# Performance work log

Hardware: AMD Instinct MI355X
Metric: run time of the kernel (lower is better)

Reference implementation:

```python
import jax, jax.numpy as jnp
import numpy as np

B, S, HID = 2, 512, 2048
HQ, HKV, D = 16, 4, 128
G = HQ // HKV
MAXP = 4096
PAST = 1536  # kv-cache start index (tokens already in cache)
EPS = 1e-6
NEG = -1e30


def _make_rope(past, s, d):
    half = d // 2
    inv_freq = 1.0 / (10000.0 ** (np.arange(half, dtype=np.float64) / half))
    pos = np.arange(past, past + s, dtype=np.float64)
    ang = pos[:, None] * inv_freq[None, :]
    return np.concatenate([np.cos(ang), np.sin(ang)], axis=-1).astype(np.float32)


def setup_inputs() -> dict:
    key = jax.random.key(0)
    ks = jax.random.split(key, 8)
    hidden_states = jax.random.normal(ks[0], (B, S, HID), jnp.float32)
    past_key_value = jax.random.normal(ks[1], (B, 2, HKV, MAXP, D), jnp.float32) * 0.5
    rope = jnp.broadcast_to(jnp.asarray(_make_rope(PAST, S, D))[None], (B, S, D))
    sc = 1.0 / np.sqrt(HID)
    Wq = jax.random.normal(ks[2], (HID, HQ * D), jnp.float32) * sc
    Wk = jax.random.normal(ks[3], (HID, HKV * D), jnp.float32) * sc
    Wv = jax.random.normal(ks[4], (HID, HKV * D), jnp.float32) * sc
    Wo = jax.random.normal(ks[5], (HQ * D, HID), jnp.float32) * (1.0 / np.sqrt(HQ * D))
    q_norm_w = jnp.ones((D,), jnp.float32)
    k_norm_w = jnp.ones((D,), jnp.float32)
    context_lengths = jnp.full((B,), PAST + S, jnp.int32)
    kvcache_start_index = jnp.full((1,), PAST, jnp.int32)
    return {"hidden_states": hidden_states, "past_key_value": past_key_value,
            "rope_rotary_cos_sin": rope, "Wq": Wq, "Wk": Wk, "Wv": Wv, "Wo": Wo,
            "q_norm_w": q_norm_w, "k_norm_w": k_norm_w,
            "context_lengths": context_lengths,
            "kvcache_start_index": kvcache_start_index}


def _rms_norm(x, w):
    # per-head RMSNorm over head_dim (Qwen3-style q_norm/k_norm)
    var = jnp.mean(jnp.square(x), axis=-1, keepdims=True)
    return x * jax.lax.rsqrt(var + EPS) * w


def _apply_rope(x, cos, sin):
    # x: [B,S,H,D]; cos/sin: [B,S,1,D/2] (neox-style half rotation)
    x1, x2 = jnp.split(x, 2, axis=-1)
    return jnp.concatenate([x1 * cos - x2 * sin, x2 * cos + x1 * sin], axis=-1)


def reference(hidden_states, past_key_value, rope_rotary_cos_sin,
              Wq, Wk, Wv, Wo, q_norm_w, k_norm_w,
              context_lengths, kvcache_start_index):
    bsz, q_len, _ = hidden_states.shape
    # QKV projections
    q = (hidden_states @ Wq).reshape(bsz, q_len, HQ, D)
    k = (hidden_states @ Wk).reshape(bsz, q_len, HKV, D)
    v = (hidden_states @ Wv).reshape(bsz, q_len, HKV, D)
    # per-head QK norm
    q = _rms_norm(q, q_norm_w)
    k = _rms_norm(k, k_norm_w)
    # RoPE (cos_sin: [B,S,D] = [cos(D/2) | sin(D/2)], fp32)
    cos = rope_rotary_cos_sin[..., : D // 2][:, :, None, :]
    sin = rope_rotary_cos_sin[..., D // 2:][:, :, None, :]
    q = _apply_rope(q, cos, sin)
    k = _apply_rope(k, cos, sin)
    # KV cache write at kvcache_start_index (in-place update, plugin semantics)
    start = kvcache_start_index[0]
    new_kv = jnp.stack([k.transpose(0, 2, 1, 3), v.transpose(0, 2, 1, 3)], axis=1)  # [B,2,HKV,S,D]
    present = jax.lax.dynamic_update_slice(
        past_key_value, new_kv.astype(past_key_value.dtype), (0, 0, 0, start, 0))
    ck = present[:, 0]  # [B,HKV,P,D]
    cv = present[:, 1]
    # GQA attention over the cache, causal w.r.t. absolute position
    qg = q.reshape(bsz, q_len, HKV, G, D).transpose(0, 2, 3, 1, 4)  # [B,HKV,G,S,D]
    scores = jnp.einsum('bhgsd,bhpd->bhgsp', qg, ck) / np.sqrt(D)
    kpos = jnp.arange(MAXP)
    limit = start + jnp.arange(q_len) + 1  # [S]: query i sees cache[0 : start+i+1]
    mask = (kpos[None, None, :] < limit[None, :, None]) & \
           (kpos[None, None, :] < context_lengths[:, None, None])  # [B,S,P]
    scores = jnp.where(mask[:, None, None], scores, NEG)
    probs = jax.nn.softmax(scores, axis=-1)
    out = jnp.einsum('bhgsp,bhpd->bhgsd', probs, cv)
    out = out.transpose(0, 3, 1, 2, 4).reshape(bsz, q_len, HQ * D)
    attn_output = out @ Wo
    return attn_output, present
```

## Files before the change

kernel.cpp:

```cpp
#include <hip/hip_runtime.h>

typedef unsigned short u16;
typedef unsigned int u32;
typedef __attribute__((ext_vector_type(4))) float f32x4;
typedef __attribute__((ext_vector_type(8))) __bf16 bf16x8;
typedef __attribute__((ext_vector_type(8))) unsigned short u16x8;

#define MAXP_ 4096
#define TOTROWS 16384
#define NCHUNK 4
#define NCALLOC 4
#define CHUNKP 512

__device__ __forceinline__ u16 f2bf(float f) {
    union { float f; u32 u; } x; x.f = f;
    u32 r = x.u + 0x7FFFu + ((x.u >> 16) & 1u);
    return (u16)(r >> 16);
}
__device__ __forceinline__ float bf2f(u16 u) {
    union { u32 u; float f; } x; x.u = ((u32)u) << 16; return x.f;
}
__device__ __forceinline__ u32 packbf(float lo, float hi) {
    return (u32)f2bf(lo) | ((u32)f2bf(hi) << 16);
}
__device__ __forceinline__ u32 bperm(int addr, u32 src) {
    return (u32)__builtin_amdgcn_ds_bpermute(addr, (int)src);
}

#define GLOAD16(g, l) __builtin_amdgcn_global_load_lds( \
    (const __attribute__((address_space(1))) void*)(g), \
    (__attribute__((address_space(3))) void*)(l), 16, 0, 0)

__global__ __launch_bounds__(256) void prep(const float* __restrict__ hidden,
        const float* __restrict__ Wq, const float* __restrict__ Wk, const float* __restrict__ Wv,
        u16* __restrict__ hb, u16* __restrict__ Wqkvt) {
    const int bid = blockIdx.x;
    const int t = threadIdx.x;
    if (bid < 1024) {
        int i = bid * 256 + t;
        const float* s = hidden + (long)i * 8;
        f32x4 a = *(const f32x4*)s;
        f32x4 b = *(const f32x4*)(s + 4);
        u16x8 o;
#pragma unroll
        for (int j = 0; j < 4; ++j) { o[j] = f2bf(a[j]); o[4 + j] = f2bf(b[j]); }
        *(u16x8*)&hb[(long)i * 8] = o;
        return;
    }
    __shared__ __align__(16) u16 T[64][72];
    const float* W; int N_w, n_off, n0, k0;
    if (bid < 2048)      { int b2 = bid - 1024; W = Wq; N_w = 2048; n_off = 0;    n0 = (b2 & 31) * 64; k0 = (b2 >> 5) * 64; }
    else if (bid < 2304) { int b2 = bid - 2048; W = Wk; N_w = 512;  n_off = 2048; n0 = (b2 & 7) * 64;  k0 = (b2 >> 3) * 64; }
    else                 { int b2 = bid - 2304; W = Wv; N_w = 512;  n_off = 2560; n0 = (b2 & 7) * 64;  k0 = (b2 >> 3) * 64; }
    {
        int r = t >> 2, c4 = (t & 3) * 16;
        const float* src = W + (long)(k0 + r) * N_w + n0 + c4;
        f32x4 a0 = *(const f32x4*)src, a1 = *(const f32x4*)(src + 4);
        f32x4 a2 = *(const f32x4*)(src + 8), a3 = *(const f32x4*)(src + 12);
        u16x8 p0, p1;
#pragma unroll
        for (int j = 0; j < 4; ++j) {
            p0[j] = f2bf(a0[j]); p0[4 + j] = f2bf(a1[j]);
            p1[j] = f2bf(a2[j]); p1[4 + j] = f2bf(a3[j]);
        }
        *(u16x8*)&T[r][c4] = p0;
        *(u16x8*)&T[r][c4 + 8] = p1;
    }
    __syncthreads();
    {
        int n = t >> 2, k4 = (t & 3) * 16;
        u16x8 q0, q1;
#pragma unroll
        for (int j = 0; j < 8; ++j) { q0[j] = T[k4 + j][n]; q1[j] = T[k4 + 8 + j][n]; }
        u16* dst = Wqkvt + (long)(n_off + n0 + n) * 2048 + k0 + k4;
        *(u16x8*)dst = q0;
        *(u16x8*)(dst + 8) = q1;
    }
}

__global__ __launch_bounds__(256) void trans_w(const float* __restrict__ W, u16* __restrict__ Wt,
                                               int N_w, int K, int n_off) {
    __shared__ __align__(16) u16 T[64][72];
    const int t = threadIdx.x;
    const int n0 = blockIdx.x * 64, k0 = blockIdx.y * 64;
    {
        int r = t >> 2, c4 = (t & 3) * 16;
        const float* src = W + (long)(k0 + r) * N_w + n0 + c4;
        f32x4 a0 = *(const f32x4*)src, a1 = *(const f32x4*)(src + 4);
        f32x4 a2 = *(const f32x4*)(src + 8), a3 = *(const f32x4*)(src + 12);
        u16x8 p0, p1;
#pragma unroll
        for (int j = 0; j < 4; ++j) {
            p0[j] = f2bf(a0[j]); p0[4 + j] = f2bf(a1[j]);
            p1[j] = f2bf(a2[j]); p1[4 + j] = f2bf(a3[j]);
        }
        *(u16x8*)&T[r][c4] = p0;
        *(u16x8*)&T[r][c4 + 8] = p1;
    }
    __syncthreads();
    {
        int n = t >> 2, k4 = (t & 3) * 16;
        u16x8 q0, q1;
#pragma unroll
        for (int j = 0; j < 8; ++j) { q0[j] = T[k4 + j][n]; q1[j] = T[k4 + 8 + j][n]; }
        u16* dst = Wt + (long)(n_off + n0 + n) * K + k0 + k4;
        *(u16x8*)dst = q0;
        *(u16x8*)(dst + 8) = q1;
    }
}

__global__ __launch_bounds__(256) void copy_past2(const float* __restrict__ past,
        float* __restrict__ present, u16* __restrict__ Kc, u16* __restrict__ Vtc,
        const int* __restrict__ startp, const int* __restrict__ ctxp) {
    __shared__ __align__(16) u16 T[128][72];
    const int bkh = blockIdx.y;
    const int b = bkh >> 3, kv = (bkh >> 2) & 1, h = bkh & 3;
    const int p0 = blockIdx.x * 64;
    const int t = threadIdx.x;
    const int p = t >> 2, d0 = (t & 3) * 32;
    const float* src = past + ((long)bkh * MAXP_ + p0 + p) * 128 + d0;
    float* dst = present + ((long)bkh * MAXP_ + p0 + p) * 128 + d0;
    f32x4 v[8];
#pragma unroll
    for (int j = 0; j < 8; ++j) { v[j] = *(const f32x4*)(src + j * 4); *(f32x4*)(dst + j * 4) = v[j]; }
    int klim = startp[0] + 512;
    int cx = ctxp[b];
    if (klim > cx) klim = cx;
    if (p0 >= klim) return;
    if (kv == 0) {
        u16* kd = Kc + ((long)(b * 4 + h) * MAXP_ + p0 + p) * 128 + d0;
#pragma unroll
        for (int j2 = 0; j2 < 4; ++j2) {
            u16x8 o;
#pragma unroll
            for (int e = 0; e < 4; ++e) { o[e] = f2bf(v[j2 * 2][e]); o[4 + e] = f2bf(v[j2 * 2 + 1][e]); }
            *(u16x8*)&kd[j2 * 8] = o;
        }
    } else {
#pragma unroll
        for (int j = 0; j < 8; ++j)
#pragma unroll
            for (int e = 0; e < 4; ++e)
                T[d0 + j * 4 + e][p] = f2bf(v[j][e]);
        __syncthreads();
        int d = t >> 1, pc = (t & 1) * 32;
        u16* vd = Vtc + ((long)(b * 4 + h) * 128 + d) * MAXP_ + p0 + pc;
#pragma unroll
        for (int j = 0; j < 4; ++j)
            *(u16x8*)&vd[j * 8] = *(const u16x8*)&T[d][pc + j * 8];
    }
}

__global__ __launch_bounds__(256) void gemm64(const u16* __restrict__ A, const u16* __restrict__ Bt,
                                              float* __restrict__ C, int M, int N, int K) {
    __shared__ __align__(16) u16 As0[4096], Bs0[4096], As1[4096], Bs1[4096];
    const int tid = threadIdx.x, lane = tid & 63, w = tid >> 6;
    const int wm = w >> 1, wn = w & 1;
    const int l15 = lane & 15, g = lane >> 4;
    const int m0 = blockIdx.y * 64, n0 = blockIdx.x * 64;
    f32x4 acc[2][2] = {};

    const int lrow = lane >> 3;
    const int sch = (lane & 7) ^ lrow;
    const int c0 = w, c1 = w + 4;
    const u16* ga0 = A + (long)(m0 + c0 * 8 + lrow) * K + sch * 8;
    const u16* ga1 = A + (long)(m0 + c1 * 8 + lrow) * K + sch * 8;
    const u16* gb0 = Bt + (long)(n0 + c0 * 8 + lrow) * K + sch * 8;
    const u16* gb1 = Bt + (long)(n0 + c1 * 8 + lrow) * K + sch * 8;
    const int ra = wm * 32, rb = wn * 32;
    const int h7 = l15 & 7;

#define STAGE_T(koff, AS_, BS_) do { \
        GLOAD16(ga0 + (koff), &AS_[c0 * 512]); \
        GLOAD16(ga1 + (koff), &AS_[c1 * 512]); \
        GLOAD16(gb0 + (koff), &BS_[c0 * 512]); \
        GLOAD16(gb1 + (koff), &BS_[c1 * 512]); \
    } while (0)

    auto compute = [&](const u16* as_, const u16* bs_) {
        bf16x8 af[2][2], bfr[2][2];
#pragma unroll
        for (int i = 0; i < 2; ++i) {
            int rr = ra + i * 16 + l15;
#pragma unroll
            for (int kk = 0; kk < 2; ++kk)
                af[i][kk] = *(const bf16x8*)&as_[rr * 64 + (((kk * 4 + g) ^ h7) * 8)];
        }
#pragma unroll
        for (int j = 0; j < 2; ++j) {
            int rr = rb + j * 16 + l15;
#pragma unroll
            for (int kk = 0; kk < 2; ++kk)
                bfr[j][kk] = *(const bf16x8*)&bs_[rr * 64 + (((kk * 4 + g) ^ h7) * 8)];
        }
#pragma unroll
        for (int i = 0; i < 2; ++i)
#pragma unroll
            for (int j = 0; j < 2; ++j) {
                acc[i][j] = __builtin_amdgcn_mfma_f32_16x16x32_bf16(af[i][0], bfr[j][0], acc[i][j], 0, 0, 0);
                acc[i][j] = __builtin_amdgcn_mfma_f32_16x16x32_bf16(af[i][1], bfr[j][1], acc[i][j], 0, 0, 0);
            }
    };

    STAGE_T(0, As0, Bs0);
    for (int k0 = 0; k0 < K; k0 += 128) {
        STAGE_T(k0 + 64, As1, Bs1);
        asm volatile("s_waitcnt vmcnt(4)" ::: "memory");
        __builtin_amdgcn_s_barrier();
        __builtin_amdgcn_sched_barrier(0);
        compute(As0, Bs0);
        __builtin_amdgcn_s_barrier();
        if (k0 + 128 < K) {
            STAGE_T(k0 + 128, As0, Bs0);
            asm volatile("s_waitcnt vmcnt(4)" ::: "memory");
        } else {
            asm volatile("s_waitcnt vmcnt(0)" ::: "memory");
        }
        __builtin_amdgcn_s_barrier();
        __builtin_amdgcn_sched_barrier(0);
        compute(As1, Bs1);
        __builtin_amdgcn_s_barrier();
    }
#undef STAGE_T

#pragma unroll
    for (int i = 0; i < 2; ++i)
#pragma unroll
        for (int j = 0; j < 2; ++j)
#pragma unroll
            for (int r = 0; r < 4; ++r)
                C[(long)(m0 + ra + i * 16 + g * 4 + r) * N + n0 + rb + j * 16 + l15] = acc[i][j][r];
}

__global__ __launch_bounds__(256) void normrope_v(const float* __restrict__ QKVf,
        const float* __restrict__ rope,
        const float* __restrict__ qw, const float* __restrict__ kw,
        const int* __restrict__ startp, float* __restrict__ present,
        u16* __restrict__ Qn, u16* __restrict__ Kc, u16* __restrict__ Vtc) {
    const int bid = blockIdx.x;
    const int start = startp[0];
    if (bid < 6144) {
        const int wid = bid * 4 + (threadIdx.x >> 6);
        const int lane = threadIdx.x & 63;
        if (wid < 16384) {
            int row = wid >> 4, h = wid & 15;
            int b = row >> 9, s = row & 511;
            const float* src = QKVf + (long)row * 3072 + h * 128;
            float x1 = src[lane], x2 = src[64 + lane];
            float v = x1 * x1 + x2 * x2;
#pragma unroll
            for (int off = 32; off; off >>= 1) v += __shfl_xor(v, off, 64);
            float sc = rsqrtf(v * (1.0f / 128.0f) + 1e-6f);
            float y1 = x1 * sc * qw[lane], y2 = x2 * sc * qw[64 + lane];
            float c = rope[(long)row * 128 + lane], sn = rope[(long)row * 128 + 64 + lane];
            u16* dst = Qn + (((long)(b * 16 + h) * 512 + s) * 128);
            dst[lane] = f2bf(y1 * c - y2 * sn);
            dst[64 + lane] = f2bf(y2 * c + y1 * sn);
        } else if (wid < 20480) {
            int j = wid - 16384;
            int row = j >> 2, h = j & 3;
            int b = row >> 9, s = row & 511;
            const float* src = QKVf + (long)row * 3072 + 2048 + h * 128;
            float x1 = src[lane], x2 = src[64 + lane];
            float v = x1 * x1 + x2 * x2;
#pragma unroll
            for (int off = 32; off; off >>= 1) v += __shfl_xor(v, off, 64);
            float sc = rsqrtf(v * (1.0f / 128.0f) + 1e-6f);
            float y1 = x1 * sc * kw[lane], y2 = x2 * sc * kw[64 + lane];
            float c = rope[(long)row * 128 + lane], sn = rope[(long)row * 128 + 64 + lane];
            float k1 = y1 * c - y2 * sn, k2 = y2 * c + y1 * sn;
            float* dst = present + (((long)(b * 2 + 0) * 4 + h) * MAXP_ + (start + s)) * 128;
            dst[lane] = k1; dst[64 + lane] = k2;
            u16* kc = Kc + (((long)(b * 4 + h)) * MAXP_ + start + s) * 128;
            kc[lane] = f2bf(k1); kc[64 + lane] = f2bf(k2);
        } else if (wid < 24576) {
            int j = wid - 20480;
            int row = j >> 2, h = j & 3;
            int b = row >> 9, s = row & 511;
            const float* src = QKVf + (long)row * 3072 + 2560 + h * 128;
            float* dst = present + (((long)(b * 2 + 1) * 4 + h) * MAXP_ + (start + s)) * 128;
            dst[lane] = src[lane];
            dst[64 + lane] = src[64 + lane];
        }
        return;
    }
    __shared__ __align__(16) u16 T[128][72];
    const int t = threadIdx.x;
    const int b2 = bid - 6144;
    const int s0 = (b2 & 7) * 64;
    const int bh = b2 >> 3, b = bh >> 2, h = bh & 3;
    const int sr = t >> 2, d0 = (t & 3) * 32;
    const float* src = QKVf + (long)(b * 512 + s0 + sr) * 3072 + 2560 + h * 128 + d0;
#pragma unroll
    for (int j = 0; j < 8; ++j) {
        f32x4 v = *(const f32x4*)(src + j * 4);
#pragma unroll
        for (int e = 0; e < 4; ++e) T[d0 + j * 4 + e][sr] = f2bf(v[e]);
    }
    __syncthreads();
    const int d = t >> 1, pc = (t & 1) * 32;
    u16* dst = Vtc + ((long)(b * 4 + h) * 128 + d) * MAXP_ + start + s0 + pc;
#pragma unroll
    for (int k = 0; k < 32; ++k) dst[k] = T[d][pc + k];
}

__global__ __launch_bounds__(512, 4) void attn(const u16* __restrict__ Qn,
        const u16* __restrict__ Kc, const u16* __restrict__ Vtc,
        const int* __restrict__ startp, const int* __restrict__ ctxp,
        u16* __restrict__ op, float* __restrict__ mp, float* __restrict__ lp) {
    __shared__ __align__(16) char KsB[2][16384];
    __shared__ __align__(16) char VsB[2][16384];
    const int tid = threadIdx.x, lane = tid & 63, w = tid >> 6;
    const int l15 = lane & 15, g = lane >> 4;
    const bool ghi = (g >= 2);
    const int id = blockIdx.x;
    const int bh = id & 7;
    const int rest = id >> 3;
    const int c = rest >> 4;
    const int q0 = (rest & 15) * 32;
    const int b = bh >> 2, hkv = bh & 3;
    const int hd = w & 3, qh = w >> 2;
    const int hq = hkv * 4 + hd;
    const int start = startp[0];
    const int ctx = ctxp[b];

    int lim_blk = start + q0 + 32;
    if (lim_blk > ctx) lim_blk = ctx;
    const int pbeg = c * CHUNKP;
    int pend = pbeg + CHUNKP;
    if (pend > lim_blk) pend = lim_blk;
    if (pbeg >= pend) return;

    const int qrow0 = q0 + qh * 16;
    const long rowbase = (long)(b * 16 + hq) * 512 + qrow0;

    bf16x8 qb[4];
    {
        const u16* qp = Qn + (rowbase + l15) * 128 + g * 8;
#pragma unroll
        for (int kf = 0; kf < 4; ++kf)
            qb[kf] = *(const bf16x8*)(qp + kf * 32);
    }

    const char* kb8 = (const char*)(Kc + (long)bh * (MAXP_ * 128));
    const char* vb8 = (const char*)(Vtc + (long)bh * (128 * MAXP_));

    const int wbase = (tid & ~63) * 16;
    auto STAGE = [&](int buf, int p0_) {
#pragma unroll
        for (int r = 0; r < 2; ++r) {
            int o_ = r * 8192 + tid * 16;
            int row = o_ >> 8;
            int colb = (o_ & 255) ^ ((row & 7) << 4);
            GLOAD16(kb8 + (long)(p0_ + row) * 256 + colb, &KsB[buf][r * 8192 + wbase]);
        }
#pragma unroll
        for (int r = 0; r < 2; ++r) {
            int o_ = r * 8192 + tid * 16;
            int row = o_ >> 7;
            int colb = (o_ & 127) ^ ((row & 7) << 4);
            GLOAD16(vb8 + (long)row * (MAXP_ * 2) + (long)p0_ * 2 + colb, &VsB[buf][r * 8192 + wbase]);
        }
    };

    f32x4 o[8] = {};
    float m_run = -1e30f, l_run = 0.f;
    int limq = start + qrow0 + l15 + 1;
    if (limq > ctx) limq = ctx;
    if (limq > pend) limq = pend;
    const int addrA = (l15 + ((g & 1) << 5)) << 2;
    const int addrB = addrA + 64;
    const float scale = 0.08838834764831845f;
    const int swz = (l15 & 7) << 4;

    const int t0 = pbeg >> 6, t1 = (pend + 63) >> 6;
    STAGE(0, t0 * 64);
    asm volatile("s_waitcnt vmcnt(0)" ::: "memory");
    __builtin_amdgcn_s_barrier();
    int cur = 0;
    for (int t = t0; t < t1; ++t) {
        const int p0 = t * 64;
        if (t + 1 < t1) STAGE(cur ^ 1, p0 + 64);
        f32x4 sacc[4] = {};
#pragma unroll
        for (int kt = 0; kt < 4; ++kt) {
            const char* krow = &KsB[cur][(kt * 16 + l15) * 256];
#pragma unroll
            for (int kf = 0; kf < 4; ++kf) {
                bf16x8 ka = *(const bf16x8*)(krow + ((kf * 64 + g * 16) ^ swz));
                sacc[kt] = __builtin_amdgcn_mfma_f32_16x16x32_bf16(ka, qb[kf], sacc[kt], 0, 0, 0);
            }
        }
        float mx = -1e30f;
#pragma unroll
        for (int kt = 0; kt < 4; ++kt)
#pragma unroll
            for (int r = 0; r < 4; ++r) {
                int key = p0 + kt * 16 + g * 4 + r;
                float x = (key < limq) ? sacc[kt][r] * scale : -1e30f;
                sacc[kt][r] = x;
                mx = fmaxf(mx, x);
            }
        mx = fmaxf(mx, __shfl_xor(mx, 16, 64));
        mx = fmaxf(mx, __shfl_xor(mx, 32, 64));
        if (!__all(mx <= m_run + 8.f)) {
            float mnew = fmaxf(m_run, mx);
            float alpha = __expf(m_run - mnew);
            m_run = mnew;
            l_run *= alpha;
            f32x4 av;
#pragma unroll
            for (int r = 0; r < 4; ++r) av[r] = __shfl(alpha, g * 4 + r, 64);
#pragma unroll
            for (int df = 0; df < 8; ++df) {
                o[df][0] *= av[0]; o[df][1] *= av[1];
                o[df][2] *= av[2]; o[df][3] *= av[3];
            }
        }
        const float mb = m_run;
        float rs = 0.f;
        u32 w0[4], w1[4];
#pragma unroll
        for (int kt = 0; kt < 4; ++kt) {
#pragma unroll
            for (int r = 0; r < 4; ++r) {
                float p = __expf(sacc[kt][r] - mb);
                sacc[kt][r] = p;
                rs += p;
            }
            w0[kt] = packbf(sacc[kt][0], sacc[kt][1]);
            w1[kt] = packbf(sacc[kt][2], sacc[kt][3]);
        }
        rs += __shfl_xor(rs, 16, 64);
        rs += __shfl_xor(rs, 32, 64);
        l_run += rs;
#pragma unroll
        for (int ks = 0; ks < 2; ++ks) {
            const int sL = 2 * ks, sH = 2 * ks + 1;
            u32 d0 = ghi ? bperm(addrA, w0[sH]) : bperm(addrA, w0[sL]);
            u32 d1 = ghi ? bperm(addrA, w1[sH]) : bperm(addrA, w1[sL]);
            u32 d2 = ghi ? bperm(addrB, w0[sH]) : bperm(addrB, w0[sL]);
            u32 d3 = ghi ? bperm(addrB, w1[sH]) : bperm(addrB, w1[sL]);
            union { u32 d[4]; bf16x8 v; } pu;
            pu.d[0] = d0; pu.d[1] = d1; pu.d[2] = d2; pu.d[3] = d3;
            bf16x8 pa = pu.v;
#pragma unroll
            for (int df = 0; df < 8; ++df) {
                const char* vrow = &VsB[cur][(df * 16 + l15) * 128];
                bf16x8 vb = *(const bf16x8*)(vrow + ((ks * 64 + g * 16) ^ swz));
                o[df] = __builtin_amdgcn_mfma_f32_16x16x32_bf16(pa, vb, o[df], 0, 0, 0);
            }
        }
        asm volatile("s_waitcnt vmcnt(0)" ::: "memory");
        __builtin_amdgcn_s_barrier();
        cur ^= 1;
    }
    {
        float invl = l_run > 0.f ? 1.0f / l_run : 0.f;
        f32x4 iv;
#pragma unroll
        for (int r = 0; r < 4; ++r) iv[r] = __shfl(invl, g * 4 + r, 64);
        u16* dst = op + ((long)c * TOTROWS + rowbase + g * 4) * 128 + l15;
#pragma unroll
        for (int r = 0; r < 4; ++r)
#pragma unroll
            for (int df = 0; df < 8; ++df)
                dst[(long)r * 128 + df * 16] = f2bf(o[df][r] * iv[r]);
        if (g == 0) {
            mp[(long)c * TOTROWS + rowbase + l15] = m_run;
            lp[(long)c * TOTROWS + rowbase + l15] = l_run;
        }
    }
}

__global__ __launch_bounds__(256) void combine(const u16* __restrict__ op,
        const float* __restrict__ mp, const float* __restrict__ lp,
        const int* __restrict__ startp, const int* __restrict__ ctxp,
        u16* __restrict__ Af) {
    const int w = threadIdx.x >> 6, lane = threadIdx.x & 63;
    const long row = (long)blockIdx.x * 4 + w;
    const int b = (int)(row >> 13), hq = ((int)row >> 9) & 15, s = (int)row & 511;
    const int start = startp[0];
    int lim = start + s + 1;
    int cx = ctxp[b];
    if (lim > cx) lim = cx;
    float mc[NCALLOC], lc[NCALLOC];
    bool has[NCALLOC];
    float M = -1e30f;
#pragma unroll
    for (int c = 0; c < NCALLOC; ++c) {
        has[c] = (c * CHUNKP < lim);
        if (has[c]) {
            mc[c] = mp[(long)c * TOTROWS + row];
            lc[c] = lp[(long)c * TOTROWS + row];
            if (lc[c] > 0.f && mc[c] > M) M = mc[c];
        }
    }
    const int d0 = lane * 2;
    float Wt = 0.f, a0 = 0.f, a1 = 0.f;
#pragma unroll
    for (int c = 0; c < NCALLOC; ++c) {
        if (has[c] && lc[c] > 0.f) {
            float wg = lc[c] * __expf(mc[c] - M);
            Wt += wg;
            u32 pr = *(const u32*)&op[((long)c * TOTROWS + row) * 128 + d0];
            a0 += wg * bf2f((u16)(pr & 0xFFFF));
            a1 += wg * bf2f((u16)(pr >> 16));
        }
    }
    float inv = 1.0f / Wt;
    u32 pk = (u32)f2bf(a0 * inv) | ((u32)f2bf(a1 * inv) << 16);
    *(u32*)&Af[((long)(b * 512 + s) * 2048) + hq * 128 + d0] = pk;
}

extern "C" void kernel_launch(void* const* d_in, const int* in_sizes, int n_in,
                              void* d_out, int out_size, void* d_ws, size_t ws_size,
                              hipStream_t stream) {
    const float* hidden = (const float*)d_in[0];
    const float* past   = (const float*)d_in[1];
    const float* rope   = (const float*)d_in[2];
    const float* Wq     = (const float*)d_in[3];
    const float* Wk     = (const float*)d_in[4];
    const float* Wv     = (const float*)d_in[5];
    const float* Wo     = (const float*)d_in[6];
    const float* qw     = (const float*)d_in[7];
    const float* kw     = (const float*)d_in[8];
    const int*   ctx    = (const int*)d_in[9];
    const int*   start  = (const int*)d_in[10];

    float* out = (float*)d_out;
    float* present = out + 2097152;
    u16* Kc = (u16*)d_out;

    char* wsb = (char*)d_ws;
    u16*   hb    = (u16*)(wsb + 0);
    u16*   Wqkvt = (u16*)(wsb + 4194304);
    float* QKVf  = (float*)(wsb + 16777216);
    u16*   op    = (u16*)(wsb + 0);
    float* mp    = (float*)(wsb + 16777216);
    float* lp    = (float*)(wsb + 17039360);
    u16*   Wot   = (u16*)(wsb + 17301504);
    u16*   Qn    = (u16*)(wsb + 29360128);
    u16*   Af    = (u16*)(wsb + 29360128);
    u16*   Vtc   = (u16*)(wsb + 33554432);

    prep<<<dim3(2560), dim3(256), 0, stream>>>(hidden, Wq, Wk, Wv, hb, Wqkvt);
    copy_past2<<<dim3(64, 16), dim3(256), 0, stream>>>(past, present, Kc, Vtc, start, ctx);
    gemm64<<<dim3(48, 16), dim3(256), 0, stream>>>(hb, Wqkvt, QKVf, 1024, 3072, 2048);
    normrope_v<<<dim3(6208), dim3(256), 0, stream>>>(QKVf, rope, qw, kw, start, present, Qn, Kc, Vtc);
    trans_w<<<dim3(32, 32), dim3(256), 0, stream>>>(Wo, Wot, 2048, 2048, 0);
    attn<<<dim3(512), dim3(512), 0, stream>>>(Qn, Kc, Vtc, start, ctx, op, mp, lp);
    combine<<<dim3(4096), dim3(256), 0, stream>>>(op, mp, lp, start, ctx, Af);
    gemm64<<<dim3(32, 16), dim3(256), 0, stream>>>(Af, Wot, out, 1024, 2048, 2048);
}
```

Measured before the change: 130.1 us.

## Fuse KV-cache copy and Wo transpose into prep; XCD-aware GEMM tile mapping

Merges the past-cache copy/convert kernel and, when the workspace is large enough, the Wo transpose into the single prep launch. This cuts kernel launches and lets these independent memory-bound jobs run concurrently. The GEMM grid is flattened to 1D and blocks are remapped so each XCD handles a contiguous set of N tiles, aiming for better L2 locality. Risks include larger per-block shared memory in prep, which can lower occupancy, and a dependence on workspace size to choose the path.

```diff
diff --git a/kernel.cpp b/kernel.cpp
--- a/kernel.cpp
+++ b/kernel.cpp
@@ -33,7 +33,10 @@
 
 __global__ __launch_bounds__(256) void prep(const float* __restrict__ hidden,
         const float* __restrict__ Wq, const float* __restrict__ Wk, const float* __restrict__ Wv,
-        u16* __restrict__ hb, u16* __restrict__ Wqkvt) {
+        const float* __restrict__ Wo, const float* __restrict__ past,
+        u16* __restrict__ hb, u16* __restrict__ Wqkvt, u16* __restrict__ Wot,
+        float* __restrict__ present, u16* __restrict__ Kc, u16* __restrict__ Vtc,
+        const int* __restrict__ startp, const int* __restrict__ ctxp) {
     const int bid = blockIdx.x;
     const int t = threadIdx.x;
     if (bid < 1024) {
@@ -47,11 +50,52 @@
         *(u16x8*)&hb[(long)i * 8] = o;
         return;
     }
+    if (bid >= 2560 && bid < 3584) {
+        __shared__ __align__(16) u16 T[128][72];
+        const int b2 = bid - 2560;
+        const int bkh = b2 >> 6;
+        const int p0 = (b2 & 63) * 64;
+        const int b = bkh >> 3, kv = (bkh >> 2) & 1, h = bkh & 3;
+        const int p = t >> 2, d0 = (t & 3) * 32;
+        const float* src = past + ((long)bkh * MAXP_ + p0 + p) * 128 + d0;
+        float* dst = present + ((long)bkh * MAXP_ + p0 + p) * 128 + d0;
+        f32x4 v[8];
+#pragma unroll
+        for (int j = 0; j < 8; ++j) { v[j] = *(const f32x4*)(src + j * 4); *(f32x4*)(dst + j * 4) = v[j]; }
+        int klim = startp[0] + 512;
+        int cx = ctxp[b];
+        if (klim > cx) klim = cx;
+        if (p0 >= klim) return;
+        if (kv == 0) {
+            u16* kd = Kc + ((long)(b * 4 + h) * MAXP_ + p0 + p) * 128 + d0;
+#pragma unroll
+            for (int j2 = 0; j2 < 4; ++j2) {
+                u16x8 o;
+#pragma unroll
+                for (int e = 0; e < 4; ++e) { o[e] = f2bf(v[j2 * 2][e]); o[4 + e] = f2bf(v[j2 * 2 + 1][e]); }
+                *(u16x8*)&kd[j2 * 8] = o;
+            }
+        } else {
+#pragma unroll
+            for (int j = 0; j < 8; ++j)
+#pragma unroll
+                for (int e = 0; e < 4; ++e)
+                    T[d0 + j * 4 + e][p] = f2bf(v[j][e]);
+            __syncthreads();
+            int d = t >> 1, pc = (t & 1) * 32;
+            u16* vd = Vtc + ((long)(b * 4 + h) * 128 + d) * MAXP_ + p0 + pc;
+#pragma unroll
+            for (int j = 0; j < 4; ++j)
+                *(u16x8*)&vd[j * 8] = *(const u16x8*)&T[d][pc + j * 8];
+        }
+        return;
+    }
     __shared__ __align__(16) u16 T[64][72];
-    const float* W; int N_w, n_off, n0, k0;
-    if (bid < 2048)      { int b2 = bid - 1024; W = Wq; N_w = 2048; n_off = 0;    n0 = (b2 & 31) * 64; k0 = (b2 >> 5) * 64; }
-    else if (bid < 2304) { int b2 = bid - 2048; W = Wk; N_w = 512;  n_off = 2048; n0 = (b2 & 7) * 64;  k0 = (b2 >> 3) * 64; }
-    else                 { int b2 = bid - 2304; W = Wv; N_w = 512;  n_off = 2560; n0 = (b2 & 7) * 64;  k0 = (b2 >> 3) * 64; }
+    const float* W; u16* Wdst; int N_w, n_off, n0, k0;
+    if (bid < 2048)      { int b2 = bid - 1024; W = Wq; Wdst = Wqkvt; N_w = 2048; n_off = 0;    n0 = (b2 & 31) * 64; k0 = (b2 >> 5) * 64; }
+    else if (bid < 2304) { int b2 = bid - 2048; W = Wk; Wdst = Wqkvt; N_w = 512;  n_off = 2048; n0 = (b2 & 7) * 64;  k0 = (b2 >> 3) * 64; }
+    else if (bid < 2560) { int b2 = bid - 2304; W = Wv; Wdst = Wqkvt; N_w = 512;  n_off = 2560; n0 = (b2 & 7) * 64;  k0 = (b2 >> 3) * 64; }
+    else                 { int b2 = bid - 3584; W = Wo; Wdst = Wot;   N_w = 2048; n_off = 0;    n0 = (b2 & 31) * 64; k0 = (b2 >> 5) * 64; }
     {
         int r = t >> 2, c4 = (t & 3) * 16;
         const float* src = W + (long)(k0 + r) * N_w + n0 + c4;
@@ -72,7 +116,7 @@
         u16x8 q0, q1;
 #pragma unroll
         for (int j = 0; j < 8; ++j) { q0[j] = T[k4 + j][n]; q1[j] = T[k4 + 8 + j][n]; }
-        u16* dst = Wqkvt + (long)(n_off + n0 + n) * 2048 + k0 + k4;
+        u16* dst = Wdst + (long)(n_off + n0 + n) * 2048 + k0 + k4;
         *(u16x8*)dst = q0;
         *(u16x8*)(dst + 8) = q1;
     }
@@ -109,55 +153,15 @@
     }
 }
 
-__global__ __launch_bounds__(256) void copy_past2(const float* __restrict__ past,
-        float* __restrict__ present, u16* __restrict__ Kc, u16* __restrict__ Vtc,
-        const int* __restrict__ startp, const int* __restrict__ ctxp) {
-    __shared__ __align__(16) u16 T[128][72];
-    const int bkh = blockIdx.y;
-    const int b = bkh >> 3, kv = (bkh >> 2) & 1, h = bkh & 3;
-    const int p0 = blockIdx.x * 64;
-    const int t = threadIdx.x;
-    const int p = t >> 2, d0 = (t & 3) * 32;
-    const float* src = past + ((long)bkh * MAXP_ + p0 + p) * 128 + d0;
-    float* dst = present + ((long)bkh * MAXP_ + p0 + p) * 128 + d0;
-    f32x4 v[8];
-#pragma unroll
-    for (int j = 0; j < 8; ++j) { v[j] = *(const f32x4*)(src + j * 4); *(f32x4*)(dst + j * 4) = v[j]; }
-    int klim = startp[0] + 512;
-    int cx = ctxp[b];
-    if (klim > cx) klim = cx;
-    if (p0 >= klim) return;
-    if (kv == 0) {
-        u16* kd = Kc + ((long)(b * 4 + h) * MAXP_ + p0 + p) * 128 + d0;
-#pragma unroll
-        for (int j2 = 0; j2 < 4; ++j2) {
-            u16x8 o;
-#pragma unroll
-            for (int e = 0; e < 4; ++e) { o[e] = f2bf(v[j2 * 2][e]); o[4 + e] = f2bf(v[j2 * 2 + 1][e]); }
-            *(u16x8*)&kd[j2 * 8] = o;
-        }
-    } else {
-#pragma unroll
-        for (int j = 0; j < 8; ++j)
-#pragma unroll
-            for (int e = 0; e < 4; ++e)
-                T[d0 + j * 4 + e][p] = f2bf(v[j][e]);
-        __syncthreads();
-        int d = t >> 1, pc = (t & 1) * 32;
-        u16* vd = Vtc + ((long)(b * 4 + h) * 128 + d) * MAXP_ + p0 + pc;
-#pragma unroll
-        for (int j = 0; j < 4; ++j)
-            *(u16x8*)&vd[j * 8] = *(const u16x8*)&T[d][pc + j * 8];
-    }
-}
-
 __global__ __launch_bounds__(256) void gemm64(const u16* __restrict__ A, const u16* __restrict__ Bt,
                                               float* __restrict__ C, int M, int N, int K) {
     __shared__ __align__(16) u16 As0[4096], Bs0[4096], As1[4096], Bs1[4096];
     const int tid = threadIdx.x, lane = tid & 63, w = tid >> 6;
     const int wm = w >> 1, wn = w & 1;
     const int l15 = lane & 15, g = lane >> 4;
-    const int m0 = blockIdx.y * 64, n0 = blockIdx.x * 64;
+    const int ntile = N >> 6, npx = ntile >> 3;
+    const int xcd = blockIdx.x & 7, j_ = blockIdx.x >> 3;
+    const int m0 = (j_ / npx) * 64, n0 = (xcd * npx + j_ % npx) * 64;
     f32x4 acc[2][2] = {};
 
     const int lrow = lane >> 3;
@@ -187,18 +191,18 @@
                 af[i][kk] = *(const bf16x8*)&as_[rr * 64 + (((kk * 4 + g) ^ h7) * 8)];
         }
 #pragma unroll
-        for (int j = 0; j < 2; ++j) {
-            int rr = rb + j * 16 + l15;
+        for (int j2 = 0; j2 < 2; ++j2) {
+            int rr = rb + j2 * 16 + l15;
 #pragma unroll
             for (int kk = 0; kk < 2; ++kk)
-                bfr[j][kk] = *(const bf16x8*)&bs_[rr * 64 + (((kk * 4 + g) ^ h7) * 8)];
+                bfr[j2][kk] = *(const bf16x8*)&bs_[rr * 64 + (((kk * 4 + g) ^ h7) * 8)];
         }
 #pragma unroll
         for (int i = 0; i < 2; ++i)
 #pragma unroll
-            for (int j = 0; j < 2; ++j) {
-                acc[i][j] = __builtin_amdgcn_mfma_f32_16x16x32_bf16(af[i][0], bfr[j][0], acc[i][j], 0, 0, 0);
-                acc[i][j] = __builtin_amdgcn_mfma_f32_16x16x32_bf16(af[i][1], bfr[j][1], acc[i][j], 0, 0, 0);
+            for (int j2 = 0; j2 < 2; ++j2) {
+                acc[i][j2] = __builtin_amdgcn_mfma_f32_16x16x32_bf16(af[i][0], bfr[j2][0], acc[i][j2], 0, 0, 0);
+                acc[i][j2] = __builtin_amdgcn_mfma_f32_16x16x32_bf16(af[i][1], bfr[j2][1], acc[i][j2], 0, 0, 0);
             }
     };
 
@@ -226,10 +230,10 @@
 #pragma unroll
     for (int i = 0; i < 2; ++i)
 #pragma unroll
-        for (int j = 0; j < 2; ++j)
+        for (int j2 = 0; j2 < 2; ++j2)
 #pragma unroll
             for (int r = 0; r < 4; ++r)
-                C[(long)(m0 + ra + i * 16 + g * 4 + r) * N + n0 + rb + j * 16 + l15] = acc[i][j][r];
+                C[(long)(m0 + ra + i * 16 + g * 4 + r) * N + n0 + rb + j2 * 16 + l15] = acc[i][j2][r];
 }
 
 __global__ __launch_bounds__(256) void normrope_v(const float* __restrict__ QKVf,
@@ -539,17 +543,28 @@
     u16*   op    = (u16*)(wsb + 0);
     float* mp    = (float*)(wsb + 16777216);
     float* lp    = (float*)(wsb + 17039360);
-    u16*   Wot   = (u16*)(wsb + 17301504);
     u16*   Qn    = (u16*)(wsb + 29360128);
     u16*   Af    = (u16*)(wsb + 29360128);
     u16*   Vtc   = (u16*)(wsb + 33554432);
-
-    prep<<<dim3(2560), dim3(256), 0, stream>>>(hidden, Wq, Wk, Wv, hb, Wqkvt);
-    copy_past2<<<dim3(64, 16), dim3(256), 0, stream>>>(past, present, Kc, Vtc, start, ctx);
-    gemm64<<<dim3(48, 16), dim3(256), 0, stream>>>(hb, Wqkvt, QKVf, 1024, 3072, 2048);
-    normrope_v<<<dim3(6208), dim3(256), 0, stream>>>(QKVf, rope, qw, kw, start, present, Qn, Kc, Vtc);
-    trans_w<<<dim3(32, 32), dim3(256), 0, stream>>>(Wo, Wot, 2048, 2048, 0);
-    attn<<<dim3(512), dim3(512), 0, stream>>>(Qn, Kc, Vtc, start, ctx, op, mp, lp);
-    combine<<<dim3(4096), dim3(256), 0, stream>>>(op, mp, lp, start, ctx, Af);
-    gemm64<<<dim3(32, 16), dim3(256), 0, stream>>>(Af, Wot, out, 1024, 2048, 2048);
-}
+    const bool bigws = (ws_size >= 50331648ull);
+    u16* Wot = bigws ? (u16*)(wsb + 41943040) : (u16*)(wsb + 17301504);
+
+    if (bigws) {
+        prep<<<dim3(4608), dim3(256), 0, stream>>>(hidden, Wq, Wk, Wv, Wo, past,
+                hb, Wqkvt, Wot, present, Kc, Vtc, start, ctx);
+        gemm64<<<dim3(768), dim3(256), 0, stream>>>(hb, Wqkvt, QKVf, 1024, 3072, 2048);
+        normrope_v<<<dim3(6208), dim3(256), 0, stream>>>(QKVf, rope, qw, kw, start, present, Qn, Kc, Vtc);
+        attn<<<dim3(512), dim3(512), 0, stream>>>(Qn, Kc, Vtc, start, ctx, op, mp, lp);
+        combine<<<dim3(4096), dim3(256), 0, stream>>>(op, mp, lp, start, ctx, Af);
+        gemm64<<<dim3(512), dim3(256), 0, stream>>>(Af, Wot, out, 1024, 2048, 2048);
+    } else {
+        prep<<<dim3(3584), dim3(256), 0, stream>>>(hidden, Wq, Wk, Wv, Wo, past,
+                hb, Wqkvt, Wot, present, Kc, Vtc, start, ctx);
+        gemm64<<<dim3(768), dim3(256), 0, stream>>>(hb, Wqkvt, QKVf, 1024, 3072, 2048);
+        normrope_v<<<dim3(6208), dim3(256), 0, stream>>>(QKVf, rope, qw, kw, start, present, Qn, Kc, Vtc);
+        trans_w<<<dim3(32, 32), dim3(256), 0, stream>>>(Wo, Wot, 2048, 2048, 0);
+        attn<<<dim3(512), dim3(512), 0, stream>>>(Qn, Kc, Vtc, start, ctx, op, mp, lp);
+        combine<<<dim3(4096), dim3(256), 0, stream>>>(op, mp, lp, start, ctx, Af);
+        gemm64<<<dim3(512), dim3(256), 0, stream>>>(Af, Wot, out, 1024, 2048, 2048);
+    }
+}
```

Measured after the change: 120.5 us. -7.4%, faster.
